# Kernel tuning notes

Measured on AMD Instinct MI355X. Metric: run time of the kernel, lower is better.

## Reference

```python
import jax, jax.numpy as jnp
import numpy as np

D_MODEL = 1024
H = 16
D_HEAD = D_MODEL // H  # 64
RANK = 32
ALPHA = 1.0


def _lora_linear(x, W, b, dW, dB):
    # merged weight: W + alpha * (dB @ dW), then x @ W_merged.T + b
    Wm = W + ALPHA * (dB @ dW)
    return x @ Wm.T + b


def setup_inputs() -> dict:
    key = jax.random.key(0)
    ks = jax.random.split(key, 20)
    inp = {"x": jax.random.normal(ks[0], (2, 2048, D_MODEL), dtype=jnp.float32)}
    i = 1
    for name in ("q", "k", "v", "o"):
        inp[f"{name}_W"] = jax.random.normal(ks[i], (D_MODEL, D_MODEL), dtype=jnp.float32) * 0.02; i += 1
        inp[f"{name}_b"] = jnp.zeros((D_MODEL,), dtype=jnp.float32)
        inp[f"{name}_dW"] = jax.random.normal(ks[i], (RANK, D_MODEL), dtype=jnp.float32) * 0.01; i += 1
        inp[f"{name}_dB"] = jax.random.normal(ks[i], (D_MODEL, RANK), dtype=jnp.float32) * 0.01; i += 1
    return inp


def reference(x, q_W, q_b, q_dW, q_dB, k_W, k_b, k_dW, k_dB,
              v_W, v_b, v_dW, v_dB, o_W, o_b, o_dW, o_dB):
    b_s, n, _ = x.shape
    # LoRA-merged QKV projections
    q = _lora_linear(x, q_W, q_b, q_dW, q_dB).reshape(b_s, n, H, D_HEAD)
    k = _lora_linear(x, k_W, k_b, k_dW, k_dB).reshape(b_s, n, H, D_HEAD)
    v = _lora_linear(x, v_W, v_b, v_dW, v_dB).reshape(b_s, n, H, D_HEAD)
    scale = 1.0 / np.sqrt(D_HEAD).astype(np.float32)
    # att: [b, h, nq, nk]
    att = jnp.einsum('bqhd,bkhd->bhqk', q, k) * scale
    att = jax.nn.softmax(att, axis=-1)  # dropout = identity (eval mode)
    out = jnp.einsum('bhqk,bkhd->bqhd', att, v).reshape(b_s, n, H * D_HEAD)
    return _lora_linear(out, o_W, o_b, o_dW, o_dB)
```

## Files before the change

kernel.cpp:

```cpp
#include <hip/hip_runtime.h>

typedef unsigned short ushort_t;
typedef unsigned int u32;
typedef __attribute__((ext_vector_type(8))) short short8;
typedef __attribute__((ext_vector_type(4))) float floatx4;

typedef const __attribute__((address_space(1))) u32* gptr_t;
typedef __attribute__((address_space(3))) u32* lptr_t;

__device__ __forceinline__ void async_copy16(void* lds, const void* g) {
  __builtin_amdgcn_global_load_lds((gptr_t)g, (lptr_t)lds, 16, 0, 0);
}

__device__ __forceinline__ ushort_t f2bf(float f) {
  u32 u = __float_as_uint(f);
  u += 0x7fffu + ((u >> 16) & 1u);
  return (ushort_t)(u >> 16);
}

__device__ __forceinline__ floatx4 mfma16(short8 a, short8 b, floatx4 c) {
  return __builtin_amdgcn_mfma_f32_16x16x32_bf16(a, b, c, 0, 0, 0);
}

struct alignas(16) F4 { float a, b, c, d; };
struct alignas(8) U4 { ushort_t a, b, c, d; };

#define QSCALE 0.18033688011112043f

__global__ __launch_bounds__(256) void split_kernel(const float* __restrict__ x,
                                                    ushort_t* __restrict__ h, int n4) {
  int i = blockIdx.x * 256 + threadIdx.x;
  if (i >= n4) return;
  F4 v = ((const F4*)x)[i];
  U4 hh = {f2bf(v.a), f2bf(v.b), f2bf(v.c), f2bf(v.d)};
  ((U4*)h)[i] = hh;
}

__global__ __launch_bounds__(256) void merge_lora(const float* __restrict__ W,
                                                  const float* __restrict__ dW,
                                                  const float* __restrict__ dB,
                                                  ushort_t* __restrict__ Wh) {
  const int ot = blockIdx.x * 8;
  const int d0 = threadIdx.x * 4;
  float acc[8][4] = {};
  for (int r = 0; r < 32; ++r) {
    F4 w = *(const F4*)&dW[r * 1024 + d0];
    float wv[4] = {w.a, w.b, w.c, w.d};
#pragma unroll
    for (int o = 0; o < 8; ++o) {
      float s = dB[(ot + o) * 32 + r];
#pragma unroll
      for (int j = 0; j < 4; ++j) acc[o][j] += s * wv[j];
    }
  }
#pragma unroll
  for (int o = 0; o < 8; ++o) {
    F4 w = *(const F4*)&W[(ot + o) * 1024 + d0];
    U4 hh = {f2bf(w.a + acc[o][0]), f2bf(w.b + acc[o][1]),
             f2bf(w.c + acc[o][2]), f2bf(w.d + acc[o][3])};
    *(U4*)&Wh[(ot + o) * 1024 + d0] = hh;
  }
}

template <int MODE>
__global__ __launch_bounds__(256) void gemm_bt(
    const ushort_t* __restrict__ A, const ushort_t* __restrict__ B,
    const float* __restrict__ b0, const float* __restrict__ b1,
    const float* __restrict__ b2,
    ushort_t* __restrict__ C, ushort_t* __restrict__ vth,
    float* __restrict__ Cf, const int M, const int N, const int K) {
  __shared__ __align__(16) ushort_t lA[128 * 32], lB[128 * 32];
  const int tid = threadIdx.x;
  const int wave = tid >> 6, lane = tid & 63;
  const int lo4 = lane & 15, quad = lane >> 4;
  const int n0 = blockIdx.x * 128, m0 = blockIdx.y * 128;
  const int wm = (wave >> 1) * 64, wn = (wave & 1) * 64;

  floatx4 acc[4][4];
  const floatx4 zero4 = {0.f, 0.f, 0.f, 0.f};
#pragma unroll
  for (int mt = 0; mt < 4; ++mt)
#pragma unroll
    for (int nt = 0; nt < 4; ++nt) acc[mt][nt] = zero4;

  const int strow = lane >> 2;
  const int stcol = (lane & 3) * 8;

  for (int kk = 0; kk < K; kk += 32) {
#pragma unroll
    for (int i = 0; i < 2; ++i) {
      const int crow = (wave * 2 + i) * 16 + strow;
      const int uoff = (wave * 2 + i) * 512;
      async_copy16(&lA[uoff], A + (size_t)(m0 + crow) * K + kk + stcol);
      async_copy16(&lB[uoff], B + (size_t)(n0 + crow) * K + kk + stcol);
    }
    __syncthreads();
    short8 a_[4], b_[4];
#pragma unroll
    for (int t = 0; t < 4; ++t) {
      a_[t] = *(const short8*)&lA[(wm + t * 16 + lo4) * 32 + quad * 8];
      b_[t] = *(const short8*)&lB[(wn + t * 16 + lo4) * 32 + quad * 8];
    }
#pragma unroll
    for (int mt = 0; mt < 4; ++mt)
#pragma unroll
      for (int nt = 0; nt < 4; ++nt) acc[mt][nt] = mfma16(a_[mt], b_[nt], acc[mt][nt]);
    __syncthreads();
  }

#pragma unroll
  for (int nt = 0; nt < 4; ++nt) {
    const int col = n0 + wn + nt * 16 + lo4;
    float bias;
    if (MODE == 0)
      bias = (col < 1024) ? b0[col] : (col < 2048) ? b1[col - 1024] : b2[col - 2048];
    else
      bias = b0[col];
#pragma unroll
    for (int mt = 0; mt < 4; ++mt)
#pragma unroll
      for (int r = 0; r < 4; ++r) {
        const int row = m0 + wm + mt * 16 + quad * 4 + r;
        float c = acc[mt][nt][r] + bias;
        if (MODE == 0) {
          if (col < 1024) c *= QSCALE;
          ushort_t hv = f2bf(c);
          if (col < 2048) {
            C[(size_t)row * 3072 + col] = hv;
          } else {
            const int d = col - 2048;
            const size_t vrow = (size_t)(((row >> 11) * 16 + (d >> 6)) * 64 + (d & 63));
            vth[vrow * 2048 + (row & 2047)] = hv;
          }
        } else {
          Cf[(size_t)row * N + col] = c;
        }
      }
  }
}

__global__ __launch_bounds__(256) void attn_kernel(
    const ushort_t* __restrict__ qkv, const ushort_t* __restrict__ vt,
    ushort_t* __restrict__ at) {
  __shared__ __align__(16) ushort_t Kh[64 * 64], Vh[64 * 64];
  __shared__ __align__(16) ushort_t P[4][16][72];
  const int qt = blockIdx.x, bh = blockIdx.y;
  const int b = bh >> 4, h = bh & 15;
  const int tid = threadIdx.x;
  const int wave = tid >> 6, lane = tid & 63;
  const int lo4 = lane & 15, quad = lane >> 4;

  short8 qh[2];
  {
    const size_t g = (size_t)(b * 2048 + qt * 64 + wave * 16 + lo4) * 3072 + h * 64 + quad * 8;
    qh[0] = *(const short8*)(qkv + g);
    qh[1] = *(const short8*)(qkv + g + 32);
  }
  float l_acc[4] = {0.f, 0.f, 0.f, 0.f};
  const floatx4 zero4 = {0.f, 0.f, 0.f, 0.f};
  floatx4 O[4];
#pragma unroll
  for (int nt = 0; nt < 4; ++nt) O[nt] = zero4;

  const int strow = lane >> 3;
  const int stcol = ((lane & 7) ^ strow) * 8;

  for (int kt = 0; kt < 32; ++kt) {
#pragma unroll
    for (int i = 0; i < 2; ++i) {
      const int row = wave * 16 + i * 8 + strow;
      const int uoff = (wave * 16 + i * 8) * 64;
      const size_t kg = (size_t)(b * 2048 + kt * 64 + row) * 3072 + 1024 + h * 64 + stcol;
      async_copy16(&Kh[uoff], qkv + kg);
      const size_t vg = (size_t)(bh * 64 + row) * 2048 + kt * 64 + stcol;
      async_copy16(&Vh[uoff], vt + vg);
    }
    __syncthreads();

    floatx4 s[4];
#pragma unroll
    for (int nt = 0; nt < 4; ++nt) s[nt] = zero4;
#pragma unroll
    for (int nt = 0; nt < 4; ++nt)
#pragma unroll
      for (int ks = 0; ks < 2; ++ks) {
        const int off = (nt * 16 + lo4) * 64 + (((ks * 4 + quad) ^ (lo4 & 7)) * 8);
        s[nt] = mfma16(qh[ks], *(const short8*)&Kh[off], s[nt]);
      }

#pragma unroll
    for (int nt = 0; nt < 4; ++nt)
#pragma unroll
      for (int r = 0; r < 4; ++r) {
        float pv = __builtin_amdgcn_exp2f(s[nt][r]);
        s[nt][r] = pv;
        P[wave][quad * 4 + r][nt * 16 + lo4] = (ushort_t)(__float_as_uint(pv) >> 16);
      }
#pragma unroll
    for (int r = 0; r < 4; ++r)
      l_acc[r] += (s[0][r] + s[1][r]) + (s[2][r] + s[3][r]);

#pragma unroll
    for (int ks = 0; ks < 2; ++ks) {
      short8 pf = *(const short8*)&P[wave][lo4][ks * 32 + quad * 8];
#pragma unroll
      for (int nt = 0; nt < 4; ++nt) {
        const int off = (nt * 16 + lo4) * 64 + (((ks * 4 + quad) ^ (lo4 & 7)) * 8);
        O[nt] = mfma16(pf, *(const short8*)&Vh[off], O[nt]);
      }
    }
    __syncthreads();
  }

  float linv[4];
#pragma unroll
  for (int r = 0; r < 4; ++r) {
    float s = l_acc[r];
    s += __shfl_xor(s, 1);
    s += __shfl_xor(s, 2);
    s += __shfl_xor(s, 4);
    s += __shfl_xor(s, 8);
    linv[r] = 1.f / s;
  }
#pragma unroll
  for (int nt = 0; nt < 4; ++nt)
#pragma unroll
    for (int r = 0; r < 4; ++r) {
      float o = O[nt][r] * linv[r];
      const size_t row = (size_t)(b * 2048 + qt * 64 + wave * 16 + quad * 4 + r);
      at[row * 1024 + h * 64 + nt * 16 + lo4] = f2bf(o);
    }
}

extern "C" void kernel_launch(void* const* d_in, const int* in_sizes, int n_in,
                              void* d_out, int out_size, void* d_ws, size_t ws_size,
                              hipStream_t stream) {
  const float* x = (const float*)d_in[0];
  const float* qW = (const float*)d_in[1];
  const float* qb = (const float*)d_in[2];
  const float* qdW = (const float*)d_in[3];
  const float* qdB = (const float*)d_in[4];
  const float* kW = (const float*)d_in[5];
  const float* kb = (const float*)d_in[6];
  const float* kdW = (const float*)d_in[7];
  const float* kdB = (const float*)d_in[8];
  const float* vW = (const float*)d_in[9];
  const float* vb = (const float*)d_in[10];
  const float* vdW = (const float*)d_in[11];
  const float* vdB = (const float*)d_in[12];
  const float* oW = (const float*)d_in[13];
  const float* ob = (const float*)d_in[14];
  const float* odW = (const float*)d_in[15];
  const float* odB = (const float*)d_in[16];

  char* ws = (char*)d_ws;
  const size_t MB = 1024u * 1024u;
  const size_t WELEM = 1024u * 1024u;
  ushort_t* xs = (ushort_t*)(ws + 0 * MB);
  ushort_t* Wm = (ushort_t*)(ws + 8 * MB);
  ushort_t* qkv = (ushort_t*)(ws + 16 * MB);
  ushort_t* vt = (ushort_t*)(ws + 40 * MB);
  ushort_t* at = xs;

  split_kernel<<<4096, 256, 0, stream>>>(x, xs, 1024 * 1024);
  merge_lora<<<128, 256, 0, stream>>>(qW, qdW, qdB, Wm + 0 * WELEM);
  merge_lora<<<128, 256, 0, stream>>>(kW, kdW, kdB, Wm + 1 * WELEM);
  merge_lora<<<128, 256, 0, stream>>>(vW, vdW, vdB, Wm + 2 * WELEM);
  merge_lora<<<128, 256, 0, stream>>>(oW, odW, odB, Wm + 3 * WELEM);

  gemm_bt<0><<<dim3(24, 32), 256, 0, stream>>>(xs, Wm, qb, kb, vb,
                                               qkv, vt, nullptr, 4096, 3072, 1024);
  attn_kernel<<<dim3(32, 32), 256, 0, stream>>>(qkv, vt, at);
  gemm_bt<1><<<dim3(8, 32), 256, 0, stream>>>(at, Wm + 3 * WELEM, ob, nullptr, nullptr,
                                              nullptr, nullptr, (float*)d_out,
                                              4096, 1024, 1024);
}
```

Measured before the change: 268.7 us.

## Split attention KV range across two wave groups, fuse prep kernels, narrow output GEMM tiles

The attention kernel now runs 512 threads per block. Two groups of four waves each process half of the key tiles, and their partial outputs and row sums are combined through shared memory at the end. The five prep kernels (input cast plus four LoRA merges) become one launch. The output-projection GEMM uses 64-wide N tiles to double its block count, and the QK buffer stride shrinks to 2048. The aim is more parallelism and occupancy for attention and the small GEMM, and fewer launches. The cost is extra shared memory and a final cross-group reduction.

```diff
diff --git a/kernel.cpp b/kernel.cpp
--- a/kernel.cpp
+++ b/kernel.cpp
@@ -27,20 +27,28 @@
 
 #define QSCALE 0.18033688011112043f
 
-__global__ __launch_bounds__(256) void split_kernel(const float* __restrict__ x,
-                                                    ushort_t* __restrict__ h, int n4) {
-  int i = blockIdx.x * 256 + threadIdx.x;
-  if (i >= n4) return;
-  F4 v = ((const F4*)x)[i];
-  U4 hh = {f2bf(v.a), f2bf(v.b), f2bf(v.c), f2bf(v.d)};
-  ((U4*)h)[i] = hh;
-}
-
-__global__ __launch_bounds__(256) void merge_lora(const float* __restrict__ W,
-                                                  const float* __restrict__ dW,
-                                                  const float* __restrict__ dB,
-                                                  ushort_t* __restrict__ Wh) {
-  const int ot = blockIdx.x * 8;
+__global__ __launch_bounds__(256) void prep_kernel(
+    const float* __restrict__ x, ushort_t* __restrict__ xs,
+    const float* __restrict__ W0, const float* __restrict__ dW0, const float* __restrict__ dB0,
+    const float* __restrict__ W1, const float* __restrict__ dW1, const float* __restrict__ dB1,
+    const float* __restrict__ W2, const float* __restrict__ dW2, const float* __restrict__ dB2,
+    const float* __restrict__ W3, const float* __restrict__ dW3, const float* __restrict__ dB3,
+    ushort_t* __restrict__ Wm) {
+  const int bid = blockIdx.x;
+  if (bid < 4096) {
+    int i = bid * 256 + threadIdx.x;
+    F4 v = ((const F4*)x)[i];
+    U4 hh = {f2bf(v.a), f2bf(v.b), f2bf(v.c), f2bf(v.d)};
+    ((U4*)xs)[i] = hh;
+    return;
+  }
+  const int t = bid - 4096;
+  const int layer = t >> 7, sub = t & 127;
+  const float* W = (layer == 0) ? W0 : (layer == 1) ? W1 : (layer == 2) ? W2 : W3;
+  const float* dW = (layer == 0) ? dW0 : (layer == 1) ? dW1 : (layer == 2) ? dW2 : dW3;
+  const float* dB = (layer == 0) ? dB0 : (layer == 1) ? dB1 : (layer == 2) ? dB2 : dB3;
+  ushort_t* Wh = Wm + (size_t)layer * 1024 * 1024;
+  const int ot = sub * 8;
   const int d0 = threadIdx.x * 4;
   float acc[8][4] = {};
   for (int r = 0; r < 32; ++r) {
@@ -62,26 +70,27 @@
   }
 }
 
-template <int MODE>
+template <int MODE, int TN>
 __global__ __launch_bounds__(256) void gemm_bt(
     const ushort_t* __restrict__ A, const ushort_t* __restrict__ B,
     const float* __restrict__ b0, const float* __restrict__ b1,
     const float* __restrict__ b2,
     ushort_t* __restrict__ C, ushort_t* __restrict__ vth,
     float* __restrict__ Cf, const int M, const int N, const int K) {
-  __shared__ __align__(16) ushort_t lA[128 * 32], lB[128 * 32];
+  constexpr int NT2 = TN / 32;
+  __shared__ __align__(16) ushort_t lA[128 * 32], lB[TN * 32];
   const int tid = threadIdx.x;
   const int wave = tid >> 6, lane = tid & 63;
   const int lo4 = lane & 15, quad = lane >> 4;
-  const int n0 = blockIdx.x * 128, m0 = blockIdx.y * 128;
-  const int wm = (wave >> 1) * 64, wn = (wave & 1) * 64;
-
-  floatx4 acc[4][4];
+  const int n0 = blockIdx.x * TN, m0 = blockIdx.y * 128;
+  const int wm = (wave >> 1) * 64, wn = (wave & 1) * (TN / 2);
+
+  floatx4 acc[4][NT2];
   const floatx4 zero4 = {0.f, 0.f, 0.f, 0.f};
 #pragma unroll
   for (int mt = 0; mt < 4; ++mt)
 #pragma unroll
-    for (int nt = 0; nt < 4; ++nt) acc[mt][nt] = zero4;
+    for (int nt = 0; nt < NT2; ++nt) acc[mt][nt] = zero4;
 
   const int strow = lane >> 2;
   const int stcol = (lane & 3) * 8;
@@ -89,27 +98,31 @@
   for (int kk = 0; kk < K; kk += 32) {
 #pragma unroll
     for (int i = 0; i < 2; ++i) {
-      const int crow = (wave * 2 + i) * 16 + strow;
-      const int uoff = (wave * 2 + i) * 512;
-      async_copy16(&lA[uoff], A + (size_t)(m0 + crow) * K + kk + stcol);
-      async_copy16(&lB[uoff], B + (size_t)(n0 + crow) * K + kk + stcol);
+      const int g = wave * 2 + i;
+      async_copy16(&lA[g * 512], A + (size_t)(m0 + g * 16 + strow) * K + kk + stcol);
+    }
+#pragma unroll
+    for (int i = 0; i < TN / 64; ++i) {
+      const int g = wave * (TN / 64) + i;
+      async_copy16(&lB[g * 512], B + (size_t)(n0 + g * 16 + strow) * K + kk + stcol);
     }
     __syncthreads();
-    short8 a_[4], b_[4];
-#pragma unroll
-    for (int t = 0; t < 4; ++t) {
+    short8 a_[4], b_[NT2];
+#pragma unroll
+    for (int t = 0; t < 4; ++t)
       a_[t] = *(const short8*)&lA[(wm + t * 16 + lo4) * 32 + quad * 8];
+#pragma unroll
+    for (int t = 0; t < NT2; ++t)
       b_[t] = *(const short8*)&lB[(wn + t * 16 + lo4) * 32 + quad * 8];
-    }
 #pragma unroll
     for (int mt = 0; mt < 4; ++mt)
 #pragma unroll
-      for (int nt = 0; nt < 4; ++nt) acc[mt][nt] = mfma16(a_[mt], b_[nt], acc[mt][nt]);
+      for (int nt = 0; nt < NT2; ++nt) acc[mt][nt] = mfma16(a_[mt], b_[nt], acc[mt][nt]);
     __syncthreads();
   }
 
 #pragma unroll
-  for (int nt = 0; nt < 4; ++nt) {
+  for (int nt = 0; nt < NT2; ++nt) {
     const int col = n0 + wn + nt * 16 + lo4;
     float bias;
     if (MODE == 0)
@@ -126,7 +139,7 @@
           if (col < 1024) c *= QSCALE;
           ushort_t hv = f2bf(c);
           if (col < 2048) {
-            C[(size_t)row * 3072 + col] = hv;
+            C[(size_t)row * 2048 + col] = hv;
           } else {
             const int d = col - 2048;
             const size_t vrow = (size_t)(((row >> 11) * 16 + (d >> 6)) * 64 + (d & 63));
@@ -139,22 +152,23 @@
   }
 }
 
-__global__ __launch_bounds__(256) void attn_kernel(
-    const ushort_t* __restrict__ qkv, const ushort_t* __restrict__ vt,
+__global__ __launch_bounds__(512) void attn_kernel(
+    const ushort_t* __restrict__ qk, const ushort_t* __restrict__ vt,
     ushort_t* __restrict__ at) {
-  __shared__ __align__(16) ushort_t Kh[64 * 64], Vh[64 * 64];
-  __shared__ __align__(16) ushort_t P[4][16][72];
+  __shared__ __align__(16) ushort_t Kh[2][64 * 64], Vh[2][64 * 64];
+  __shared__ __align__(16) ushort_t P[8][16][72];
   const int qt = blockIdx.x, bh = blockIdx.y;
   const int b = bh >> 4, h = bh & 15;
   const int tid = threadIdx.x;
   const int wave = tid >> 6, lane = tid & 63;
+  const int half = wave >> 2, w4 = wave & 3;
   const int lo4 = lane & 15, quad = lane >> 4;
 
   short8 qh[2];
   {
-    const size_t g = (size_t)(b * 2048 + qt * 64 + wave * 16 + lo4) * 3072 + h * 64 + quad * 8;
-    qh[0] = *(const short8*)(qkv + g);
-    qh[1] = *(const short8*)(qkv + g + 32);
+    const size_t g = (size_t)(b * 2048 + qt * 64 + w4 * 16 + lo4) * 2048 + h * 64 + quad * 8;
+    qh[0] = *(const short8*)(qk + g);
+    qh[1] = *(const short8*)(qk + g + 32);
   }
   float l_acc[4] = {0.f, 0.f, 0.f, 0.f};
   const floatx4 zero4 = {0.f, 0.f, 0.f, 0.f};
@@ -165,15 +179,16 @@
   const int strow = lane >> 3;
   const int stcol = ((lane & 7) ^ strow) * 8;
 
-  for (int kt = 0; kt < 32; ++kt) {
+  for (int it = 0; it < 16; ++it) {
+    const int kt = half * 16 + it;
 #pragma unroll
     for (int i = 0; i < 2; ++i) {
-      const int row = wave * 16 + i * 8 + strow;
-      const int uoff = (wave * 16 + i * 8) * 64;
-      const size_t kg = (size_t)(b * 2048 + kt * 64 + row) * 3072 + 1024 + h * 64 + stcol;
-      async_copy16(&Kh[uoff], qkv + kg);
+      const int row = w4 * 16 + i * 8 + strow;
+      const int uoff = (w4 * 16 + i * 8) * 64;
+      const size_t kg = (size_t)(b * 2048 + kt * 64 + row) * 2048 + 1024 + h * 64 + stcol;
+      async_copy16(&Kh[half][uoff], qk + kg);
       const size_t vg = (size_t)(bh * 64 + row) * 2048 + kt * 64 + stcol;
-      async_copy16(&Vh[uoff], vt + vg);
+      async_copy16(&Vh[half][uoff], vt + vg);
     }
     __syncthreads();
 
@@ -185,7 +200,7 @@
 #pragma unroll
       for (int ks = 0; ks < 2; ++ks) {
         const int off = (nt * 16 + lo4) * 64 + (((ks * 4 + quad) ^ (lo4 & 7)) * 8);
-        s[nt] = mfma16(qh[ks], *(const short8*)&Kh[off], s[nt]);
+        s[nt] = mfma16(qh[ks], *(const short8*)&Kh[half][off], s[nt]);
       }
 
 #pragma unroll
@@ -206,13 +221,12 @@
 #pragma unroll
       for (int nt = 0; nt < 4; ++nt) {
         const int off = (nt * 16 + lo4) * 64 + (((ks * 4 + quad) ^ (lo4 & 7)) * 8);
-        O[nt] = mfma16(pf, *(const short8*)&Vh[off], O[nt]);
+        O[nt] = mfma16(pf, *(const short8*)&Vh[half][off], O[nt]);
       }
     }
     __syncthreads();
   }
 
-  float linv[4];
 #pragma unroll
   for (int r = 0; r < 4; ++r) {
     float s = l_acc[r];
@@ -220,16 +234,37 @@
     s += __shfl_xor(s, 2);
     s += __shfl_xor(s, 4);
     s += __shfl_xor(s, 8);
-    linv[r] = 1.f / s;
-  }
-#pragma unroll
-  for (int nt = 0; nt < 4; ++nt)
-#pragma unroll
-    for (int r = 0; r < 4; ++r) {
-      float o = O[nt][r] * linv[r];
-      const size_t row = (size_t)(b * 2048 + qt * 64 + wave * 16 + quad * 4 + r);
-      at[row * 1024 + h * 64 + nt * 16 + lo4] = f2bf(o);
-    }
+    l_acc[r] = s;
+  }
+
+  float* Om = (float*)&Kh[0][0];
+  float* Lm = (float*)&Vh[0][0];
+  if (half == 1) {
+#pragma unroll
+    for (int nt = 0; nt < 4; ++nt)
+#pragma unroll
+      for (int r = 0; r < 4; ++r)
+        Om[(w4 * 16 + quad * 4 + r) * 64 + nt * 16 + lo4] = O[nt][r];
+    if (lo4 == 0) {
+#pragma unroll
+      for (int r = 0; r < 4; ++r) Lm[w4 * 16 + quad * 4 + r] = l_acc[r];
+    }
+  }
+  __syncthreads();
+  if (half == 0) {
+    float linv[4];
+#pragma unroll
+    for (int r = 0; r < 4; ++r)
+      linv[r] = 1.f / (l_acc[r] + Lm[w4 * 16 + quad * 4 + r]);
+#pragma unroll
+    for (int nt = 0; nt < 4; ++nt)
+#pragma unroll
+      for (int r = 0; r < 4; ++r) {
+        float o = (O[nt][r] + Om[(w4 * 16 + quad * 4 + r) * 64 + nt * 16 + lo4]) * linv[r];
+        const size_t row = (size_t)(b * 2048 + qt * 64 + w4 * 16 + quad * 4 + r);
+        at[row * 1024 + h * 64 + nt * 16 + lo4] = f2bf(o);
+      }
+  }
 }
 
 extern "C" void kernel_launch(void* const* d_in, const int* in_sizes, int n_in,
@@ -258,20 +293,16 @@
   const size_t WELEM = 1024u * 1024u;
   ushort_t* xs = (ushort_t*)(ws + 0 * MB);
   ushort_t* Wm = (ushort_t*)(ws + 8 * MB);
-  ushort_t* qkv = (ushort_t*)(ws + 16 * MB);
-  ushort_t* vt = (ushort_t*)(ws + 40 * MB);
+  ushort_t* qk = (ushort_t*)(ws + 16 * MB);
+  ushort_t* vt = (ushort_t*)(ws + 32 * MB);
   ushort_t* at = xs;
 
-  split_kernel<<<4096, 256, 0, stream>>>(x, xs, 1024 * 1024);
-  merge_lora<<<128, 256, 0, stream>>>(qW, qdW, qdB, Wm + 0 * WELEM);
-  merge_lora<<<128, 256, 0, stream>>>(kW, kdW, kdB, Wm + 1 * WELEM);
-  merge_lora<<<128, 256, 0, stream>>>(vW, vdW, vdB, Wm + 2 * WELEM);
-  merge_lora<<<128, 256, 0, stream>>>(oW, odW, odB, Wm + 3 * WELEM);
-
-  gemm_bt<0><<<dim3(24, 32), 256, 0, stream>>>(xs, Wm, qb, kb, vb,
-                                               qkv, vt, nullptr, 4096, 3072, 1024);
-  attn_kernel<<<dim3(32, 32), 256, 0, stream>>>(qkv, vt, at);
-  gemm_bt<1><<<dim3(8, 32), 256, 0, stream>>>(at, Wm + 3 * WELEM, ob, nullptr, nullptr,
-                                              nullptr, nullptr, (float*)d_out,
-                                              4096, 1024, 1024);
-}
+  prep_kernel<<<4608, 256, 0, stream>>>(x, xs, qW, qdW, qdB, kW, kdW, kdB,
+                                        vW, vdW, vdB, oW, odW, odB, Wm);
+  gemm_bt<0, 128><<<dim3(24, 32), 256, 0, stream>>>(xs, Wm, qb, kb, vb,
+                                                    qk, vt, nullptr, 4096, 3072, 1024);
+  attn_kernel<<<dim3(32, 32), 512, 0, stream>>>(qk, vt, at);
+  gemm_bt<1, 64><<<dim3(16, 32), 256, 0, stream>>>(at, Wm + 3 * WELEM, ob, nullptr,
+                                                   nullptr, nullptr, nullptr,
+                                                   (float*)d_out, 4096, 1024, 1024);
+}
```

Result: faster. 247.0 us (-8.0%).
